# Performance work log

Hardware: AMD Instinct MI355X
Metric: run time of the kernel (lower is better)

The kernel has to match this reference:

```python
import jax, jax.numpy as jnp
import numpy as np

N_POINTS = 16384
N_SAMPLES = 8192


def setup_inputs() -> dict:
    key = jax.random.key(0)
    k1, k2, k3, k4 = jax.random.split(key, 4)
    a = jax.random.normal(k1, (3, N_POINTS), dtype=jnp.float32)
    b = jax.random.normal(k2, (3, N_POINTS), dtype=jnp.float32)
    # stand-ins for np.random.shuffle(...)[:n_samples] in the torch forward
    a_idx = jax.random.randint(k3, (N_SAMPLES,), 0, N_POINTS, dtype=jnp.int64)
    b_idx = jax.random.randint(k4, (N_SAMPLES,), 0, N_POINTS, dtype=jnp.int64)
    return {"a": a, "b": b, "a_idx": a_idx, "b_idx": b_idx}


def reference(a, b, a_idx, b_idx):
    # a, b: [3, N]; sample n_samples columns, transpose -> [n, 3], keep xyz
    pa = a[:, a_idx].T[:, :3]  # [n, 3]
    pb = b[:, b_idx].T[:, :3]  # [n, 3]
    # d[k, i] = ||pa_i - pb_k||^2, via ||a||^2 + ||b||^2 - 2 b.a^T
    # (avoids the original's [n, n, 3] broadcasted difference tensor)
    sq_a = jnp.sum(pa * pa, axis=1)  # [n]
    sq_b = jnp.sum(pb * pb, axis=1)  # [n]
    d = sq_a[None, :] + sq_b[:, None] - 2.0 * (pb @ pa.T)  # [n, n]
    # torch.min(d, 0)[0].sum(): min over b-points for each a-point, then sum
    return jnp.min(d, axis=0).sum()
```

## Files before the change

kernel.cpp:

```cpp
#include <hip/hip_runtime.h>
#include <stdint.h>


#define MT    256
#define APB   16
#define NPA   4
#define CH    1024
#define NCH   8
#define CPAD  (CH + CH / 16)

__global__ __launch_bounds__(128)
void chamfer_pack_kernel(const float* __restrict__ a,
                         const float* __restrict__ b,
                         const int* __restrict__ a_idx,
                         const int* __restrict__ b_idx,
                         float4* __restrict__ pa4,
                         float4* __restrict__ pb4,
                         float* __restrict__ out,
                         int N, int n) {
    int i = blockIdx.x * 128 + threadIdx.x;
    if (i < n) {
        int ai = a_idx[i];
        float x = a[ai], y = a[N + ai], z = a[2 * N + ai];
        pa4[i] = make_float4(x, y, z, x * x + y * y + z * z);
        int bi = b_idx[i];
        float u = b[bi], v = b[N + bi], w = b[2 * N + bi];
        pb4[i] = make_float4(-2.f * u, -2.f * v, -2.f * w,
                             u * u + v * v + w * w);
    }
    if (i == 0) out[0] = 0.f;
}

__global__ __launch_bounds__(MT)
void chamfer_min_kernel(const float4* __restrict__ pa4,
                        const float4* __restrict__ pb4,
                        float* __restrict__ out) {
    __shared__ float4 tile[2][CPAD];
    __shared__ float  red[4][APB];

    const int t = threadIdx.x;
    const int g = t & 3;
    const int s = t >> 2;
    const int abase = blockIdx.x * APB;

    float ax[NPA], ay[NPA], az[NPA], mn[NPA];
#pragma unroll
    for (int m = 0; m < NPA; ++m) {
        float4 p = pa4[abase + g * NPA + m];
        ax[m] = p.x; ay[m] = p.y; az[m] = p.z;
        mn[m] = 3.4e38f;
    }

    float4 r0 = pb4[t], r1 = pb4[t + 256], r2 = pb4[t + 512], r3 = pb4[t + 768];

    for (int c = 0; c < NCH; ++c) {
        float4* tl = tile[c & 1];
        {
            int u;
            u = t;        tl[u + (u >> 4)] = r0;
            u = t + 256;  tl[u + (u >> 4)] = r1;
            u = t + 512;  tl[u + (u >> 4)] = r2;
            u = t + 768;  tl[u + (u >> 4)] = r3;
        }
        __syncthreads();
        if (c + 1 < NCH) {
            const float4* src = pb4 + (c + 1) * CH;
            r0 = src[t]; r1 = src[t + 256]; r2 = src[t + 512]; r3 = src[t + 768];
        }
        const float4* row = &tl[s * 17];
#pragma unroll
        for (int j = 0; j < 16; ++j) {
            float4 bt = row[j];
#pragma unroll
            for (int m = 0; m < NPA; ++m) {
                float d = fmaf(bt.x, ax[m],
                          fmaf(bt.y, ay[m],
                          fmaf(bt.z, az[m], bt.w)));
                mn[m] = fminf(mn[m], d);
            }
        }
    }

#pragma unroll
    for (int m = 0; m < NPA; ++m) {
        float v = mn[m];
        v = fminf(v, __shfl_xor(v, 4, 64));
        v = fminf(v, __shfl_xor(v, 8, 64));
        v = fminf(v, __shfl_xor(v, 16, 64));
        v = fminf(v, __shfl_xor(v, 32, 64));
        mn[m] = v;
    }
    if ((t & 63) < 4) {
#pragma unroll
        for (int m = 0; m < NPA; ++m)
            red[t >> 6][(t & 3) * NPA + m] = mn[m];
    }
    __syncthreads();
    if (t < APB) {
        float v = fminf(fminf(red[0][t], red[1][t]),
                        fminf(red[2][t], red[3][t]));
        v += pa4[abase + t].w;
        v += __shfl_down(v, 8, 16);
        v += __shfl_down(v, 4, 16);
        v += __shfl_down(v, 2, 16);
        v += __shfl_down(v, 1, 16);
        if (t == 0) atomicAdd(out, v);
    }
}

extern "C" void kernel_launch(void* const* d_in, const int* in_sizes, int n_in,
                              void* d_out, int out_size, void* d_ws, size_t ws_size,
                              hipStream_t stream) {
    const float* a     = (const float*)d_in[0];
    const float* b     = (const float*)d_in[1];
    const int*   a_idx = (const int*)d_in[2];
    const int*   b_idx = (const int*)d_in[3];
    float*       out   = (float*)d_out;

    const int N = in_sizes[0] / 3;
    const int n = in_sizes[2];

    float4* pa4 = (float4*)d_ws;
    float4* pb4 = pa4 + n;

    chamfer_pack_kernel<<<n / 128, 128, 0, stream>>>(
        a, b, a_idx, b_idx, pa4, pb4, out, N, n);

    chamfer_min_kernel<<<n / APB, MT, 0, stream>>>(pa4, pb4, out);
}
```

Measured before the change: 75.78 us.

## Stream B points from global directly and finish with a last-block ticket reduction

Removes the LDS double-buffered B tile. Each thread now reads B points straight from global memory, which is L2-resident, and compares them against 8 A points held in registers per block instead of 4 per thread. The float atomicAdd into the output is replaced by per-block partial sums plus a ticket counter, so the last block to finish does a deterministic final reduction. This cuts LDS traffic and barriers, but it doubles the grid size, reloads all of B once per block of 8 A points, and adds a serial tail to the reduction.

New measurement: 95.81 us. 26.4% more time.

```diff
diff --git a/kernel.cpp b/kernel.cpp
--- a/kernel.cpp
+++ b/kernel.cpp
@@ -3,11 +3,7 @@
 
 
 #define MT    256
-#define APB   16
-#define NPA   4
-#define CH    1024
-#define NCH   8
-#define CPAD  (CH + CH / 16)
+#define APB   8
 
 __global__ __launch_bounds__(128)
 void chamfer_pack_kernel(const float* __restrict__ a,
@@ -16,7 +12,7 @@
                          const int* __restrict__ b_idx,
                          float4* __restrict__ pa4,
                          float4* __restrict__ pb4,
-                         float* __restrict__ out,
+                         unsigned* __restrict__ ticket,
                          int N, int n) {
     int i = blockIdx.x * 128 + threadIdx.x;
     if (i < n) {
@@ -28,83 +24,94 @@
         pb4[i] = make_float4(-2.f * u, -2.f * v, -2.f * w,
                              u * u + v * v + w * w);
     }
-    if (i == 0) out[0] = 0.f;
+    if (i == 0)
+        __hip_atomic_store(ticket, 0u, __ATOMIC_RELEASE,
+                           __HIP_MEMORY_SCOPE_AGENT);
 }
 
 __global__ __launch_bounds__(MT)
 void chamfer_min_kernel(const float4* __restrict__ pa4,
                         const float4* __restrict__ pb4,
-                        float* __restrict__ out) {
-    __shared__ float4 tile[2][CPAD];
-    __shared__ float  red[4][APB];
+                        float* __restrict__ partial,
+                        unsigned* __restrict__ ticket,
+                        float* __restrict__ out,
+                        int n) {
+    __shared__ float red[4][APB];
+    __shared__ int   lastflag;
 
-    const int t = threadIdx.x;
-    const int g = t & 3;
-    const int s = t >> 2;
-    const int abase = blockIdx.x * APB;
+    const int t     = threadIdx.x;
+    const int bid   = blockIdx.x;
+    const int abase = bid * APB;
 
-    float ax[NPA], ay[NPA], az[NPA], mn[NPA];
+    float ax[APB], ay[APB], az[APB], mn[APB];
 #pragma unroll
-    for (int m = 0; m < NPA; ++m) {
-        float4 p = pa4[abase + g * NPA + m];
+    for (int m = 0; m < APB; ++m) {
+        float4 p = pa4[abase + m];
         ax[m] = p.x; ay[m] = p.y; az[m] = p.z;
         mn[m] = 3.4e38f;
     }
 
-    float4 r0 = pb4[t], r1 = pb4[t + 256], r2 = pb4[t + 512], r3 = pb4[t + 768];
-
-    for (int c = 0; c < NCH; ++c) {
-        float4* tl = tile[c & 1];
-        {
-            int u;
-            u = t;        tl[u + (u >> 4)] = r0;
-            u = t + 256;  tl[u + (u >> 4)] = r1;
-            u = t + 512;  tl[u + (u >> 4)] = r2;
-            u = t + 768;  tl[u + (u >> 4)] = r3;
-        }
-        __syncthreads();
-        if (c + 1 < NCH) {
-            const float4* src = pb4 + (c + 1) * CH;
-            r0 = src[t]; r1 = src[t + 256]; r2 = src[t + 512]; r3 = src[t + 768];
-        }
-        const float4* row = &tl[s * 17];
+    const int NJ = n >> 8;
+#pragma unroll 4
+    for (int j = 0; j < NJ; ++j) {
+        float4 bt = pb4[j * MT + t];
 #pragma unroll
-        for (int j = 0; j < 16; ++j) {
-            float4 bt = row[j];
-#pragma unroll
-            for (int m = 0; m < NPA; ++m) {
-                float d = fmaf(bt.x, ax[m],
-                          fmaf(bt.y, ay[m],
-                          fmaf(bt.z, az[m], bt.w)));
-                mn[m] = fminf(mn[m], d);
-            }
+        for (int m = 0; m < APB; ++m) {
+            float d = fmaf(bt.x, ax[m],
+                      fmaf(bt.y, ay[m],
+                      fmaf(bt.z, az[m], bt.w)));
+            mn[m] = fminf(mn[m], d);
         }
     }
 
 #pragma unroll
-    for (int m = 0; m < NPA; ++m) {
+    for (int m = 0; m < APB; ++m) {
         float v = mn[m];
+        v = fminf(v, __shfl_xor(v, 1, 64));
+        v = fminf(v, __shfl_xor(v, 2, 64));
         v = fminf(v, __shfl_xor(v, 4, 64));
         v = fminf(v, __shfl_xor(v, 8, 64));
         v = fminf(v, __shfl_xor(v, 16, 64));
         v = fminf(v, __shfl_xor(v, 32, 64));
-        mn[m] = v;
-    }
-    if ((t & 63) < 4) {
-#pragma unroll
-        for (int m = 0; m < NPA; ++m)
-            red[t >> 6][(t & 3) * NPA + m] = mn[m];
+        if ((t & 63) == m) red[t >> 6][m] = v;
     }
     __syncthreads();
+
+    float bp = 0.f;
     if (t < APB) {
         float v = fminf(fminf(red[0][t], red[1][t]),
                         fminf(red[2][t], red[3][t]));
         v += pa4[abase + t].w;
-        v += __shfl_down(v, 8, 16);
-        v += __shfl_down(v, 4, 16);
-        v += __shfl_down(v, 2, 16);
-        v += __shfl_down(v, 1, 16);
-        if (t == 0) atomicAdd(out, v);
+        v += __shfl_down(v, 4, 8);
+        v += __shfl_down(v, 2, 8);
+        v += __shfl_down(v, 1, 8);
+        bp = v;
+    }
+
+    if (t == 0) {
+        __hip_atomic_store(&partial[bid], bp, __ATOMIC_RELEASE,
+                           __HIP_MEMORY_SCOPE_AGENT);
+        unsigned old = __hip_atomic_fetch_add(ticket, 1u, __ATOMIC_ACQ_REL,
+                                              __HIP_MEMORY_SCOPE_AGENT);
+        lastflag = (old == gridDim.x - 1);
+    }
+    __syncthreads();
+
+    if (lastflag) {
+        float s = 0.f;
+        for (int i = t; i < (int)gridDim.x; i += MT)
+            s += __hip_atomic_load(&partial[i], __ATOMIC_ACQUIRE,
+                                   __HIP_MEMORY_SCOPE_AGENT);
+        s += __shfl_xor(s, 1, 64);
+        s += __shfl_xor(s, 2, 64);
+        s += __shfl_xor(s, 4, 64);
+        s += __shfl_xor(s, 8, 64);
+        s += __shfl_xor(s, 16, 64);
+        s += __shfl_xor(s, 32, 64);
+        if ((t & 63) == 0) red[t >> 6][0] = s;
+        __syncthreads();
+        if (t == 0)
+            out[0] = red[0][0] + red[1][0] + red[2][0] + red[3][0];
     }
 }
 
@@ -120,11 +127,14 @@
     const int N = in_sizes[0] / 3;
     const int n = in_sizes[2];
 
-    float4* pa4 = (float4*)d_ws;
-    float4* pb4 = pa4 + n;
+    float4*   pa4     = (float4*)d_ws;
+    float4*   pb4     = pa4 + n;
+    float*    partial = (float*)(pb4 + n);
+    unsigned* ticket  = (unsigned*)(partial + n / APB);
 
     chamfer_pack_kernel<<<n / 128, 128, 0, stream>>>(
-        a, b, a_idx, b_idx, pa4, pb4, out, N, n);
+        a, b, a_idx, b_idx, pa4, pb4, ticket, N, n);
 
-    chamfer_min_kernel<<<n / APB, MT, 0, stream>>>(pa4, pb4, out);
+    chamfer_min_kernel<<<n / APB, MT, 0, stream>>>(
+        pa4, pb4, partial, ticket, out, n);
 }
```
